# Optimization experiments

Hardware: AMD Instinct MI355X
Metric: run time of the kernel (lower is better)

Reference implementation:

```python
import jax, jax.numpy as jnp
import numpy as np

D_MODEL = 1024
NUM_HEADS = 16
D_HEAD = D_MODEL // NUM_HEADS
ROPE_BASE = 10000.0


def _rope(x):
    # x: (B, H, S, Dh); lucidrains interleaved rotary along seq dim
    dh = x.shape[-1]
    s = x.shape[-2]
    inv_freq = 1.0 / (ROPE_BASE ** (jnp.arange(0, dh, 2, dtype=jnp.float32) / dh))
    freqs = jnp.arange(s, dtype=jnp.float32)[:, None] * inv_freq[None, :]  # (S, Dh/2)
    cos = jnp.repeat(jnp.cos(freqs), 2, axis=-1)  # (S, Dh), [f0,f0,f1,f1,...]
    sin = jnp.repeat(jnp.sin(freqs), 2, axis=-1)
    x1 = x[..., ::2]
    x2 = x[..., 1::2]
    rot = jnp.stack([-x2, x1], axis=-1).reshape(x.shape)  # rotate_half, interleaved
    return x * cos + rot * sin


def setup_inputs() -> dict:
    key = jax.random.key(0)
    ks = jax.random.split(key, 16)
    B, S, D, H, Dh = 8, 1024, D_MODEL, NUM_HEADS, D_HEAD
    scale = 1.0 / np.sqrt(D)
    inp = {
        "query": jax.random.normal(ks[0], (B, S, D), jnp.float32),
        "key": jax.random.normal(ks[1], (B, S, D), jnp.float32),
        "value": jax.random.normal(ks[2], (B, S, D), jnp.float32),
        "mask": jax.random.randint(ks[3], (B, S, S), 0, 2).astype(bool),
        "Wq": jax.random.normal(ks[4], (D, D), jnp.float32) * scale,
        "bq": jnp.zeros((D,), jnp.float32),
        "Wk": jax.random.normal(ks[5], (D, D), jnp.float32) * scale,
        "bk": jnp.zeros((D,), jnp.float32),
        "Wv": jax.random.normal(ks[6], (D, D), jnp.float32) * scale,
        "bv": jnp.zeros((D,), jnp.float32),
        "u_bias": jax.random.normal(ks[7], (H, Dh), jnp.float32) * (1.0 / np.sqrt(Dh)),
        "Wo": jax.random.normal(ks[8], (D, D), jnp.float32) * scale,
        "bo": jnp.zeros((D,), jnp.float32),
    }
    return inp


def reference(query, key, value, mask, Wq, bq, Wk, bk, Wv, bv, u_bias, Wo, bo):
    B, S, D = query.shape
    H, Dh = NUM_HEADS, D_HEAD
    # projections -> (B, H, S, Dh)
    q = (query @ Wq.T + bq).reshape(B, S, H, Dh).transpose(0, 2, 1, 3)
    k = (key @ Wk.T + bk).reshape(B, S, H, Dh).transpose(0, 2, 1, 3)
    v = (value @ Wv.T + bv).reshape(B, S, H, Dh).transpose(0, 2, 1, 3)
    q = _rope(q)  # (B, H, S, Dh)
    k = _rope(k)
    # (q + u_bias) @ k^T ; u_bias broadcasts over (H, Dh)
    qb = q + u_bias[None, :, None, :]
    score = jnp.einsum("bhsd,bhtd->bhst", qb, k) / np.sqrt(Dh)
    score = jnp.where(mask[:, None, :, :], -1e9, score)
    attn = jax.nn.softmax(score, axis=-1)  # dropout is identity in eval mode
    ctx = jnp.einsum("bhst,bhtd->bhsd", attn, v)  # (B, H, S, Dh)
    ctx = ctx.transpose(0, 2, 1, 3).reshape(B, S, D)
    return ctx @ Wo.T + bo
```

## Files before the change

### kernel.cpp

```cpp
#include <hip/hip_runtime.h>

#define S_LEN 1024
#define D_MODELX 1024
#define NHEAD 16
#define DHEAD 64
#define BATCH 8
#define NTOK (BATCH * S_LEN)

typedef __bf16 bf16;
typedef __attribute__((ext_vector_type(8))) __bf16 bf16x8;
typedef __attribute__((ext_vector_type(4))) __bf16 bf16x4;
typedef __attribute__((ext_vector_type(4))) float f32x4;

__device__ __forceinline__ void gload_lds16(const void* gsrc, void* ldst) {
  __builtin_amdgcn_global_load_lds(
      (const __attribute__((address_space(1))) void*)gsrc,
      (__attribute__((address_space(3))) void*)ldst,
      16, 0, 0);
}

__global__ __launch_bounds__(256) void rope_tables(float* __restrict__ cosT,
                                                   float* __restrict__ sinT) {
  int idx = blockIdx.x * 256 + threadIdx.x;
  int s = idx >> 5;
  int i = idx & 31;
  float inv = powf(10000.0f, -(float)i / 32.0f);
  float f = (float)s * inv;
  cosT[idx] = cosf(f);
  sinT[idx] = sinf(f);
}

__global__ __launch_bounds__(256) void cvt4(const float* __restrict__ in,
                                            bf16* __restrict__ out, int n4) {
  int i = blockIdx.x * 256 + threadIdx.x;
  if (i < n4) {
    float4 v = ((const float4*)in)[i];
    bf16x4 o;
    o[0] = (bf16)v.x; o[1] = (bf16)v.y; o[2] = (bf16)v.z; o[3] = (bf16)v.w;
    ((bf16x4*)out)[i] = o;
  }
}

template <int MODE>
__global__ __launch_bounds__(256) void gemm_bt(
    const bf16* __restrict__ X, const bf16* __restrict__ W,
    const float* __restrict__ bias, void* __restrict__ outp,
    const float* __restrict__ cosT, const float* __restrict__ sinT,
    const float* __restrict__ ubias) {
  __shared__ bf16 At[128 * 32];
  __shared__ bf16 Bt[128 * 32];
  const int tid = threadIdx.x;
  const int lane = tid & 63;
  const int wid = tid >> 6;
  const int m0 = blockIdx.x * 128;
  const int n0 = blockIdx.y * 128;
  const int g = lane >> 4;
  const int li = lane & 15;
  const int wr = (wid >> 1) * 64;
  const int wc = (wid & 1) * 64;

  f32x4 acc[4][4] = {};

  for (int k0 = 0; k0 < D_MODELX; k0 += 32) {
    __syncthreads();
#pragma unroll
    for (int c = 0; c < 2; ++c) {
      int chunk = wid * 128 + c * 64 + lane;
      int r = chunk >> 2;
      int seg = chunk & 3;
      gload_lds16(X + (size_t)(m0 + r) * D_MODELX + k0 + seg * 8,
                  &At[(wid * 128 + c * 64) * 8]);
      gload_lds16(W + (size_t)(n0 + r) * D_MODELX + k0 + seg * 8,
                  &Bt[(wid * 128 + c * 64) * 8]);
    }
    __syncthreads();
    bf16x8 af[4], bfr[4];
#pragma unroll
    for (int m = 0; m < 4; ++m)
      af[m] = *(const bf16x8*)&At[(wr + m * 16 + li) * 32 + g * 8];
#pragma unroll
    for (int n = 0; n < 4; ++n)
      bfr[n] = *(const bf16x8*)&Bt[(wc + n * 16 + li) * 32 + g * 8];
#pragma unroll
    for (int m = 0; m < 4; ++m)
#pragma unroll
      for (int n = 0; n < 4; ++n)
        acc[m][n] = __builtin_amdgcn_mfma_f32_16x16x32_bf16(af[m], bfr[n],
                                                            acc[m][n], 0, 0, 0);
  }

#pragma unroll
  for (int m = 0; m < 4; ++m) {
#pragma unroll
    for (int n = 0; n < 4; ++n) {
      int col = n0 + wc + n * 16 + li;
#pragma unroll
      for (int rg = 0; rg < 4; ++rg) {
        int token = m0 + wr + m * 16 + g * 4 + rg;
        float v = acc[m][n][rg] + bias[col];
        if (MODE <= 1) {
          float p = __shfl_xor(v, 1, 64);
          int s = token & (S_LEN - 1);
          int b = token >> 10;
          int dh = col & 63;
          int h = col >> 6;
          int fi = dh >> 1;
          float cv = cosT[s * 32 + fi];
          float sv = sinT[s * 32 + fi];
          float vr = (dh & 1) ? (v * cv + p * sv) : (v * cv - p * sv);
          if (MODE == 0) vr += ubias[(h << 6) + dh];
          ((bf16*)outp)[(((size_t)b * NHEAD + h) * S_LEN + s) * DHEAD + dh] = (bf16)vr;
        } else if (MODE == 2) {
          int s = token & (S_LEN - 1);
          int b = token >> 10;
          int dh = col & 63;
          int h = col >> 6;
          ((bf16*)outp)[(((size_t)b * NHEAD + h) * S_LEN + s) * DHEAD + dh] = (bf16)v;
        } else {
          ((float*)outp)[(size_t)token * D_MODELX + col] = v;
        }
      }
    }
  }
}

__global__ __launch_bounds__(256) void attn_fwd(
    const bf16* __restrict__ Q, const bf16* __restrict__ K,
    const bf16* __restrict__ V, const int* __restrict__ mask,
    bf16* __restrict__ ctx) {
  __shared__ bf16 Kl[64 * 72];
  __shared__ bf16 Vt[64 * 72];
  __shared__ bf16 Pl[4][16 * 72];

  const int tid = threadIdx.x;
  const int lane = tid & 63;
  const int wid = tid >> 6;
  const int bh = blockIdx.y;
  const int qblk = blockIdx.x;
  const int b = bh >> 4;
  const int h = bh & 15;
  const int g = lane >> 4;
  const int li = lane & 15;
  const int q0 = qblk * 64 + wid * 16;

  const bf16* qbase = Q + ((size_t)bh * S_LEN + q0) * DHEAD;
  bf16x8 qf[2];
  qf[0] = *(const bf16x8*)&qbase[(size_t)li * DHEAD + g * 8];
  qf[1] = *(const bf16x8*)&qbase[(size_t)li * DHEAD + 32 + g * 8];

  f32x4 ctxacc[4] = {};
  float mrun[4], lrun[4];
#pragma unroll
  for (int rg = 0; rg < 4; ++rg) { mrun[rg] = -INFINITY; lrun[rg] = 0.0f; }

  const int* mrow = mask + (size_t)b * S_LEN * S_LEN + (size_t)q0 * S_LEN;

  for (int t0 = 0; t0 < S_LEN; t0 += 64) {
    __syncthreads();
#pragma unroll
    for (int j = 0; j < 2; ++j) {
      int c = tid + j * 256;
      int r = c >> 3;
      int seg = c & 7;
      bf16x8 kv = *(const bf16x8*)&K[((size_t)bh * S_LEN + t0 + r) * DHEAD + seg * 8];
      *(bf16x8*)&Kl[r * 72 + seg * 8] = kv;
      bf16x8 vv = *(const bf16x8*)&V[((size_t)bh * S_LEN + t0 + r) * DHEAD + seg * 8];
#pragma unroll
      for (int e = 0; e < 8; ++e) Vt[(seg * 8 + e) * 72 + r] = vv[e];
    }
    __syncthreads();

    f32x4 sc[4];
#pragma unroll
    for (int tt = 0; tt < 4; ++tt) {
      f32x4 a = {};
      bf16x8 kf0 = *(const bf16x8*)&Kl[(tt * 16 + li) * 72 + g * 8];
      bf16x8 kf1 = *(const bf16x8*)&Kl[(tt * 16 + li) * 72 + 32 + g * 8];
      a = __builtin_amdgcn_mfma_f32_16x16x32_bf16(qf[0], kf0, a, 0, 0, 0);
      a = __builtin_amdgcn_mfma_f32_16x16x32_bf16(qf[1], kf1, a, 0, 0, 0);
      sc[tt] = a;
    }

    float pm[4][4];
    float chmax[4];
#pragma unroll
    for (int rg = 0; rg < 4; ++rg) chmax[rg] = -INFINITY;
#pragma unroll
    for (int tt = 0; tt < 4; ++tt) {
      int t = tt * 16 + li;
#pragma unroll
      for (int rg = 0; rg < 4; ++rg) {
        float s = sc[tt][rg] * 0.125f;
        if (mrow[(size_t)(g * 4 + rg) * S_LEN + t0 + t]) s = -1.0e9f;
        pm[tt][rg] = s;
        chmax[rg] = fmaxf(chmax[rg], s);
      }
    }
#pragma unroll
    for (int sft = 1; sft < 16; sft <<= 1)
#pragma unroll
      for (int rg = 0; rg < 4; ++rg)
        chmax[rg] = fmaxf(chmax[rg], __shfl_xor(chmax[rg], sft, 64));

    float corr[4], csum[4];
#pragma unroll
    for (int rg = 0; rg < 4; ++rg) {
      float mnew = fmaxf(mrun[rg], chmax[rg]);
      corr[rg] = __expf(mrun[rg] - mnew);
      mrun[rg] = mnew;
      csum[rg] = 0.0f;
    }
#pragma unroll
    for (int tt = 0; tt < 4; ++tt)
#pragma unroll
      for (int rg = 0; rg < 4; ++rg) {
        float p = __expf(pm[tt][rg] - mrun[rg]);
        pm[tt][rg] = p;
        csum[rg] += p;
      }
#pragma unroll
    for (int sft = 1; sft < 16; sft <<= 1)
#pragma unroll
      for (int rg = 0; rg < 4; ++rg)
        csum[rg] += __shfl_xor(csum[rg], sft, 64);
#pragma unroll
    for (int rg = 0; rg < 4; ++rg) lrun[rg] = lrun[rg] * corr[rg] + csum[rg];

#pragma unroll
    for (int tt = 0; tt < 4; ++tt)
#pragma unroll
      for (int rg = 0; rg < 4; ++rg)
        Pl[wid][(g * 4 + rg) * 72 + tt * 16 + li] = (bf16)pm[tt][rg];

#pragma unroll
    for (int dd = 0; dd < 4; ++dd)
#pragma unroll
      for (int rg = 0; rg < 4; ++rg) ctxacc[dd][rg] *= corr[rg];

#pragma unroll
    for (int sub = 0; sub < 2; ++sub) {
      bf16x8 pf = *(const bf16x8*)&Pl[wid][li * 72 + sub * 32 + g * 8];
#pragma unroll
      for (int dd = 0; dd < 4; ++dd) {
        bf16x8 vf = *(const bf16x8*)&Vt[(dd * 16 + li) * 72 + sub * 32 + g * 8];
        ctxacc[dd] = __builtin_amdgcn_mfma_f32_16x16x32_bf16(pf, vf, ctxacc[dd], 0, 0, 0);
      }
    }
  }

#pragma unroll
  for (int dd = 0; dd < 4; ++dd)
#pragma unroll
    for (int rg = 0; rg < 4; ++rg) {
      float vout = ctxacc[dd][rg] / lrun[rg];
      int s = q0 + g * 4 + rg;
      int d = h * 64 + dd * 16 + li;
      ctx[((size_t)b * S_LEN + s) * D_MODELX + d] = (bf16)vout;
    }
}

extern "C" void kernel_launch(void* const* d_in, const int* in_sizes, int n_in,
                              void* d_out, int out_size, void* d_ws, size_t ws_size,
                              hipStream_t stream) {
  const float* query = (const float*)d_in[0];
  const float* key   = (const float*)d_in[1];
  const float* value = (const float*)d_in[2];
  const int*   mask  = (const int*)d_in[3];
  const float* Wq = (const float*)d_in[4];
  const float* bq = (const float*)d_in[5];
  const float* Wk = (const float*)d_in[6];
  const float* bk = (const float*)d_in[7];
  const float* Wv = (const float*)d_in[8];
  const float* bv = (const float*)d_in[9];
  const float* ub = (const float*)d_in[10];
  const float* Wo = (const float*)d_in[11];
  const float* bo = (const float*)d_in[12];
  float* out = (float*)d_out;

  char* wsb = (char*)d_ws;
  size_t off = 0;
  auto give = [&](size_t bytes) -> char* {
    char* p = wsb + off;
    off += bytes;
    return p;
  };
  const size_t ACT = (size_t)NTOK * D_MODELX * 2;
  const size_t WB  = (size_t)D_MODELX * D_MODELX * 2;
  bf16* Xq   = (bf16*)give(ACT);
  bf16* Xk   = (bf16*)give(ACT);
  bf16* Xv   = (bf16*)give(ACT);
  bf16* Wqb  = (bf16*)give(WB);
  bf16* Wkb  = (bf16*)give(WB);
  bf16* Wvb  = (bf16*)give(WB);
  bf16* Wob  = (bf16*)give(WB);
  bf16* qws  = (bf16*)give(ACT);
  bf16* kws  = (bf16*)give(ACT);
  bf16* vws  = (bf16*)give(ACT);
  float* cosT = (float*)give((size_t)S_LEN * 32 * 4);
  float* sinT = (float*)give((size_t)S_LEN * 32 * 4);
  bf16* ctxw = Xq;

  rope_tables<<<128, 256, 0, stream>>>(cosT, sinT);

  const int actN4 = NTOK * D_MODELX / 4;
  const int wN4   = D_MODELX * D_MODELX / 4;
  cvt4<<<actN4 / 256, 256, 0, stream>>>(query, Xq, actN4);
  cvt4<<<actN4 / 256, 256, 0, stream>>>(key,   Xk, actN4);
  cvt4<<<actN4 / 256, 256, 0, stream>>>(value, Xv, actN4);
  cvt4<<<wN4 / 256, 256, 0, stream>>>(Wq, Wqb, wN4);
  cvt4<<<wN4 / 256, 256, 0, stream>>>(Wk, Wkb, wN4);
  cvt4<<<wN4 / 256, 256, 0, stream>>>(Wv, Wvb, wN4);
  cvt4<<<wN4 / 256, 256, 0, stream>>>(Wo, Wob, wN4);

  dim3 ggrid(NTOK / 128, D_MODELX / 128);
  gemm_bt<0><<<ggrid, 256, 0, stream>>>(Xq, Wqb, bq, qws, cosT, sinT, ub);
  gemm_bt<1><<<ggrid, 256, 0, stream>>>(Xk, Wkb, bk, kws, cosT, sinT, ub);
  gemm_bt<2><<<ggrid, 256, 0, stream>>>(Xv, Wvb, bv, vws, cosT, sinT, ub);

  dim3 agrid(S_LEN / 64, BATCH * NHEAD);
  attn_fwd<<<agrid, 256, 0, stream>>>(qws, kws, vws, mask, ctxw);

  gemm_bt<3><<<ggrid, 256, 0, stream>>>(ctxw, Wob, bo, out, cosT, sinT, ub);
}
```

Baseline: 462.5 us.

## Pack mask to bits, pre-transpose V, double-buffer K/V with async LDS loads

Adds a ballot-based kernel that packs the int mask into 64-bit words, so the attention kernel reads 1 bit per element instead of 4 bytes. The V projection epilogue now writes V transposed (per head, d-major), which removes the scalar LDS transpose in attention. K/V tiles are double-buffered with global_load_lds direct-to-LDS copies and XOR-swizzled layouts in place of padding. The cost is one extra full pass over the 32MB mask plus the risks that come with the swizzle and async-wait logic.

After: 440.7 us. 4.7% less time.

```diff
diff --git a/kernel.cpp b/kernel.cpp
--- a/kernel.cpp
+++ b/kernel.cpp
@@ -39,6 +39,13 @@
     o[0] = (bf16)v.x; o[1] = (bf16)v.y; o[2] = (bf16)v.z; o[3] = (bf16)v.w;
     ((bf16x4*)out)[i] = o;
   }
+}
+
+__global__ __launch_bounds__(256) void maskpack(const int* __restrict__ m,
+                                                unsigned long long* __restrict__ out) {
+  int i = blockIdx.x * 256 + threadIdx.x;
+  unsigned long long bal = __ballot(m[i] != 0);
+  if ((threadIdx.x & 63) == 0) out[i >> 6] = bal;
 }
 
 template <int MODE>
@@ -94,30 +101,36 @@
 #pragma unroll
     for (int n = 0; n < 4; ++n) {
       int col = n0 + wc + n * 16 + li;
-#pragma unroll
-      for (int rg = 0; rg < 4; ++rg) {
-        int token = m0 + wr + m * 16 + g * 4 + rg;
-        float v = acc[m][n][rg] + bias[col];
-        if (MODE <= 1) {
-          float p = __shfl_xor(v, 1, 64);
-          int s = token & (S_LEN - 1);
-          int b = token >> 10;
-          int dh = col & 63;
-          int h = col >> 6;
-          int fi = dh >> 1;
-          float cv = cosT[s * 32 + fi];
-          float sv = sinT[s * 32 + fi];
-          float vr = (dh & 1) ? (v * cv + p * sv) : (v * cv - p * sv);
-          if (MODE == 0) vr += ubias[(h << 6) + dh];
-          ((bf16*)outp)[(((size_t)b * NHEAD + h) * S_LEN + s) * DHEAD + dh] = (bf16)vr;
-        } else if (MODE == 2) {
-          int s = token & (S_LEN - 1);
-          int b = token >> 10;
-          int dh = col & 63;
-          int h = col >> 6;
-          ((bf16*)outp)[(((size_t)b * NHEAD + h) * S_LEN + s) * DHEAD + dh] = (bf16)v;
-        } else {
-          ((float*)outp)[(size_t)token * D_MODELX + col] = v;
+      if (MODE == 2) {
+        int token0 = m0 + wr + m * 16 + g * 4;
+        int s0 = token0 & (S_LEN - 1);
+        int b0 = token0 >> 10;
+        int dh = col & 63;
+        int h = col >> 6;
+        bf16x4 o;
+#pragma unroll
+        for (int rg = 0; rg < 4; ++rg) o[rg] = (bf16)(acc[m][n][rg] + bias[col]);
+        *(bf16x4*)&((bf16*)outp)[(((size_t)b0 * NHEAD + h) * DHEAD + dh) * S_LEN + s0] = o;
+      } else {
+#pragma unroll
+        for (int rg = 0; rg < 4; ++rg) {
+          int token = m0 + wr + m * 16 + g * 4 + rg;
+          float v = acc[m][n][rg] + bias[col];
+          if (MODE <= 1) {
+            float p = __shfl_xor(v, 1, 64);
+            int s = token & (S_LEN - 1);
+            int b = token >> 10;
+            int dh = col & 63;
+            int h = col >> 6;
+            int fi = dh >> 1;
+            float cv = cosT[s * 32 + fi];
+            float sv = sinT[s * 32 + fi];
+            float vr = (dh & 1) ? (v * cv + p * sv) : (v * cv - p * sv);
+            if (MODE == 0) vr += ubias[(h << 6) + dh];
+            ((bf16*)outp)[(((size_t)b * NHEAD + h) * S_LEN + s) * DHEAD + dh] = (bf16)vr;
+          } else {
+            ((float*)outp)[(size_t)token * D_MODELX + col] = v;
+          }
         }
       }
     }
@@ -126,11 +139,11 @@
 
 __global__ __launch_bounds__(256) void attn_fwd(
     const bf16* __restrict__ Q, const bf16* __restrict__ K,
-    const bf16* __restrict__ V, const int* __restrict__ mask,
+    const bf16* __restrict__ V, const unsigned long long* __restrict__ mp,
     bf16* __restrict__ ctx) {
-  __shared__ bf16 Kl[64 * 72];
-  __shared__ bf16 Vt[64 * 72];
-  __shared__ bf16 Pl[4][16 * 72];
+  __shared__ bf16 Kl[2][64 * 64];
+  __shared__ bf16 Vt[2][64 * 64];
+  __shared__ bf16 Pl[4][16 * 64];
 
   const int tid = threadIdx.x;
   const int lane = tid & 63;
@@ -153,45 +166,61 @@
 #pragma unroll
   for (int rg = 0; rg < 4; ++rg) { mrun[rg] = -INFINITY; lrun[rg] = 0.0f; }
 
-  const int* mrow = mask + (size_t)b * S_LEN * S_LEN + (size_t)q0 * S_LEN;
-
-  for (int t0 = 0; t0 < S_LEN; t0 += 64) {
-    __syncthreads();
+  const bf16* gk = K + (size_t)bh * S_LEN * DHEAD;
+  const bf16* gv = V + (size_t)bh * DHEAD * S_LEN;
+  const unsigned long long* mrowp = mp + ((size_t)b * S_LEN + q0) * 16;
+
+  const int srow = lane >> 3;
+  const int schunk = (lane & 7) ^ srow;
+
+  auto stage = [&](int bi, int it) {
+    int t0 = it * 64;
 #pragma unroll
     for (int j = 0; j < 2; ++j) {
-      int c = tid + j * 256;
-      int r = c >> 3;
-      int seg = c & 7;
-      bf16x8 kv = *(const bf16x8*)&K[((size_t)bh * S_LEN + t0 + r) * DHEAD + seg * 8];
-      *(bf16x8*)&Kl[r * 72 + seg * 8] = kv;
-      bf16x8 vv = *(const bf16x8*)&V[((size_t)bh * S_LEN + t0 + r) * DHEAD + seg * 8];
-#pragma unroll
-      for (int e = 0; e < 8; ++e) Vt[(seg * 8 + e) * 72 + r] = vv[e];
-    }
-    __syncthreads();
+      int row = wid * 16 + j * 8 + srow;
+      gload_lds16(gk + ((size_t)(t0 + row)) * DHEAD + schunk * 8,
+                  &Kl[bi][(wid * 16 + j * 8) * 64]);
+      gload_lds16(gv + (size_t)row * S_LEN + t0 + schunk * 8,
+                  &Vt[bi][(wid * 16 + j * 8) * 64]);
+    }
+  };
+
+  stage(0, 0);
+  int buf = 0;
+
+  for (int it = 0; it < S_LEN / 64; ++it) {
+    asm volatile("s_waitcnt vmcnt(0)" ::: "memory");
+    __builtin_amdgcn_s_barrier();
+    if (it + 1 < S_LEN / 64) stage(buf ^ 1, it + 1);
 
     f32x4 sc[4];
 #pragma unroll
     for (int tt = 0; tt < 4; ++tt) {
+      int row = tt * 16 + li;
+      int sz = li & 7;
+      bf16x8 kf0 = *(const bf16x8*)&Kl[buf][row * 64 + ((g ^ sz) << 3)];
+      bf16x8 kf1 = *(const bf16x8*)&Kl[buf][row * 64 + (((g + 4) ^ sz) << 3)];
       f32x4 a = {};
-      bf16x8 kf0 = *(const bf16x8*)&Kl[(tt * 16 + li) * 72 + g * 8];
-      bf16x8 kf1 = *(const bf16x8*)&Kl[(tt * 16 + li) * 72 + 32 + g * 8];
       a = __builtin_amdgcn_mfma_f32_16x16x32_bf16(qf[0], kf0, a, 0, 0, 0);
       a = __builtin_amdgcn_mfma_f32_16x16x32_bf16(qf[1], kf1, a, 0, 0, 0);
       sc[tt] = a;
     }
 
+    unsigned long long mw[4];
+#pragma unroll
+    for (int rg = 0; rg < 4; ++rg)
+      mw[rg] = mrowp[(size_t)(g * 4 + rg) * 16 + it];
+
     float pm[4][4];
     float chmax[4];
 #pragma unroll
     for (int rg = 0; rg < 4; ++rg) chmax[rg] = -INFINITY;
 #pragma unroll
     for (int tt = 0; tt < 4; ++tt) {
-      int t = tt * 16 + li;
 #pragma unroll
       for (int rg = 0; rg < 4; ++rg) {
         float s = sc[tt][rg] * 0.125f;
-        if (mrow[(size_t)(g * 4 + rg) * S_LEN + t0 + t]) s = -1.0e9f;
+        if ((mw[rg] >> (tt * 16 + li)) & 1ull) s = -1.0e9f;
         pm[tt][rg] = s;
         chmax[rg] = fmaxf(chmax[rg], s);
       }
@@ -229,8 +258,11 @@
 #pragma unroll
     for (int tt = 0; tt < 4; ++tt)
 #pragma unroll
-      for (int rg = 0; rg < 4; ++rg)
-        Pl[wid][(g * 4 + rg) * 72 + tt * 16 + li] = (bf16)pm[tt][rg];
+      for (int rg = 0; rg < 4; ++rg) {
+        int q = g * 4 + rg;
+        int t = tt * 16 + li;
+        Pl[wid][q * 64 + (t ^ ((q & 7) << 3))] = (bf16)pm[tt][rg];
+      }
 
 #pragma unroll
     for (int dd = 0; dd < 4; ++dd)
@@ -239,13 +271,15 @@
 
 #pragma unroll
     for (int sub = 0; sub < 2; ++sub) {
-      bf16x8 pf = *(const bf16x8*)&Pl[wid][li * 72 + sub * 32 + g * 8];
+      bf16x8 pf = *(const bf16x8*)&Pl[wid][li * 64 + (((sub * 4 + g) ^ (li & 7)) << 3)];
 #pragma unroll
       for (int dd = 0; dd < 4; ++dd) {
-        bf16x8 vf = *(const bf16x8*)&Vt[(dd * 16 + li) * 72 + sub * 32 + g * 8];
+        int row = dd * 16 + li;
+        bf16x8 vf = *(const bf16x8*)&Vt[buf][row * 64 + (((sub * 4 + g) ^ (row & 7)) << 3)];
         ctxacc[dd] = __builtin_amdgcn_mfma_f32_16x16x32_bf16(pf, vf, ctxacc[dd], 0, 0, 0);
       }
     }
+    buf ^= 1;
   }
 
 #pragma unroll
@@ -281,7 +315,7 @@
   size_t off = 0;
   auto give = [&](size_t bytes) -> char* {
     char* p = wsb + off;
-    off += bytes;
+    off += (bytes + 255) & ~(size_t)255;
     return p;
   };
   const size_t ACT = (size_t)NTOK * D_MODELX * 2;
@@ -296,11 +330,13 @@
   bf16* qws  = (bf16*)give(ACT);
   bf16* kws  = (bf16*)give(ACT);
   bf16* vws  = (bf16*)give(ACT);
+  unsigned long long* mp = (unsigned long long*)give((size_t)BATCH * S_LEN * 16 * 8);
   float* cosT = (float*)give((size_t)S_LEN * 32 * 4);
   float* sinT = (float*)give((size_t)S_LEN * 32 * 4);
   bf16* ctxw = Xq;
 
   rope_tables<<<128, 256, 0, stream>>>(cosT, sinT);
+  maskpack<<<(BATCH * S_LEN * S_LEN) / 256, 256, 0, stream>>>(mask, mp);
 
   const int actN4 = NTOK * D_MODELX / 4;
   const int wN4   = D_MODELX * D_MODELX / 4;
@@ -318,7 +354,7 @@
   gemm_bt<2><<<ggrid, 256, 0, stream>>>(Xv, Wvb, bv, vws, cosT, sinT, ub);
 
   dim3 agrid(S_LEN / 64, BATCH * NHEAD);
-  attn_fwd<<<agrid, 256, 0, stream>>>(qws, kws, vws, mask, ctxw);
+  attn_fwd<<<agrid, 256, 0, stream>>>(qws, kws, vws, mp, ctxw);
 
   gemm_bt<3><<<ggrid, 256, 0, stream>>>(ctxw, Wob, bo, out, cosT, sinT, ub);
 }
```
